# Kernel tuning notes

Hardware: AMD Instinct MI355X
Metric: run time of the kernel (lower is better)

The kernel has to match this reference:

```python
import jax, jax.numpy as jnp
import numpy as np

WS = 7   # w_size
K = 9    # k_neighbors


def setup_inputs() -> dict:
    key = jax.random.key(0)
    ks = jax.random.split(key, 6)
    B, C, H, W = 16, 64, 112, 112
    Cf = C // 4
    return {
        'x_in': jax.random.normal(ks[0], (B, C, H, W), jnp.float32),
        'Wf': jax.random.normal(ks[1], (Cf, C), jnp.float32) / np.sqrt(C).astype(np.float32),
        'bf': jnp.zeros((Cf,), jnp.float32),
        'Wp': jax.random.normal(ks[2], (C, Cf), jnp.float32) / np.sqrt(Cf).astype(np.float32),
        'bp': jnp.zeros((C,), jnp.float32),
        'W1': jax.random.normal(ks[3], (4, 2), jnp.float32) / np.sqrt(2.0).astype(np.float32),
        'b1': jnp.zeros((4,), jnp.float32),
        'W2': jax.random.normal(ks[4], (1, 4), jnp.float32) / 2.0,
        'b2': jnp.zeros((1,), jnp.float32),
        'sigma': jnp.asarray(4.0, jnp.float32),
        'alpha': jnp.asarray(0.5, jnp.float32),
    }


def reference(x_in, Wf, bf, Wp, bp, W1, b1, W2, b2, sigma, alpha):
    B, C, H, W = x_in.shape
    w, h = H // WS, W // WS                      # per-window spatial dims
    Bp, N = B * WS * WS, w * h                   # num windows, nodes per window
    # window partition: b c (Wg w) (Hg h) -> (b Wg Hg) c w h
    x = x_in.reshape(B, C, WS, w, WS, h).transpose(0, 2, 4, 1, 3, 5).reshape(Bp, C, w, h)
    # 1x1 conv f: dim -> dim//4
    f = jnp.einsum('bchw,oc->bohw', x, Wf) + bf[None, :, None, None]
    Cf = f.shape[1]
    xf = f.reshape(Bp, Cf, N).transpose(0, 2, 1)          # [Bp, N, Cf] node features
    # all-pairs cosine similarity (torch eps=1e-8)
    xn = xf / jnp.maximum(jnp.linalg.norm(xf, axis=-1, keepdims=True), 1e-8)
    sim_feat = jnp.einsum('bnc,bmc->bnm', xn, xn)         # [Bp, N, N]
    # spatial gaussian similarity
    ii, jj = jnp.meshgrid(jnp.arange(w), jnp.arange(h), indexing='ij')
    coords = jnp.stack([ii, jj], -1).reshape(N, 2).astype(jnp.float32)
    dist = jnp.sqrt(jnp.sum((coords[:, None] - coords[None]) ** 2, -1))
    sim_dist = jnp.exp(-dist ** 2 / (2.0 * sigma ** 2))   # [N, N]
    combined = alpha * sim_feat + (1.0 - alpha) * sim_dist[None]
    _, idx = jax.lax.top_k(combined, K)                   # [Bp, N, K] neighbor ids
    # gather neighbor messages; edges of node n are exactly its K top-k columns
    msg = xf[jnp.arange(Bp)[:, None, None], idx]          # [Bp, N, K, Cf]
    sf = jnp.take_along_axis(sim_feat, idx, axis=-1)      # edge cosine sim
    sd = sim_dist[jnp.arange(N)[:, None], idx]            # edge spatial sim
    pair = jnp.stack([sf, sd], -1)                        # [Bp, N, K, 2]
    hdn = jax.nn.silu(pair @ W1.T + b1)
    wgt = jax.nn.sigmoid(hdn @ W2.T + b2)[..., 0]         # [Bp, N, K]
    # scatter_add over edge_index[0] == per-source sum over its K edges
    wn = wgt / (jnp.sum(wgt, -1, keepdims=True) + 1e-12)
    out = jnp.einsum('bnk,bnkc->bnc', wn, msg)            # [Bp, N, Cf]
    out = out.reshape(Bp, w, h, Cf).transpose(0, 3, 1, 2)
    # window un-partition: (b Wg Hg) c w h -> b c (Wg w) (Hg h)
    out = out.reshape(B, WS, WS, Cf, w, h).transpose(0, 3, 1, 4, 2, 5).reshape(B, Cf, H, W)
    # 1x1 conv p: dim//4 -> dim, then flatten(2)
    y = jnp.einsum('bchw,oc->bohw', out, Wp) + bp[None, :, None, None]
    return y.reshape(B, C, H * W)
```

## Files before the change

kernel.cpp:

```cpp
#include <hip/hip_runtime.h>
#include <math.h>

#define CC    64
#define CF    16
#define NPIX  256
#define KK    9
#define HWQ   12544
#define WWQ   112
#define NTILE 784

__global__ __launch_bounds__(64, 4) void feat_k(
    const float* __restrict__ x_in, const float* __restrict__ Wf,
    const float* __restrict__ bf,
    float* __restrict__ xn_g, float* __restrict__ nrm_g)
{
    __shared__ float s_Wt[CC * CF];
    __shared__ float s_bf[CF];
    const int tid = threadIdx.x;
    for (int idx = tid; idx < CC * CF; idx += 64) {
        int c = idx >> 4, o = idx & 15;
        s_Wt[idx] = Wf[o * CC + c];
    }
    if (tid < CF) s_bf[tid] = bf[tid];
    __syncthreads();

    const int p    = blockIdx.x * 64 + tid;
    const int tile = p >> 8, pix = p & 255;
    const int bb = tile / 49, ssb = tile % 49;
    const int s1 = ssb / 7, s2 = ssb % 7;
    const int gy = s1 * 16 + (pix >> 4), gx = s2 * 16 + (pix & 15);
    const float* xb = x_in + (size_t)bb * CC * HWQ + (size_t)gy * WWQ + gx;

    float fv[CF];
    #pragma unroll
    for (int o = 0; o < CF; ++o) fv[o] = 0.0f;
    #pragma unroll 4
    for (int c = 0; c < CC; ++c) {
        float xv = xb[(size_t)c * HWQ];
        const float4* w4 = reinterpret_cast<const float4*>(&s_Wt[c << 4]);
        float4 w0 = w4[0], w1 = w4[1], w2 = w4[2], w3 = w4[3];
        fv[0]  = fmaf(xv, w0.x, fv[0]);  fv[1]  = fmaf(xv, w0.y, fv[1]);
        fv[2]  = fmaf(xv, w0.z, fv[2]);  fv[3]  = fmaf(xv, w0.w, fv[3]);
        fv[4]  = fmaf(xv, w1.x, fv[4]);  fv[5]  = fmaf(xv, w1.y, fv[5]);
        fv[6]  = fmaf(xv, w1.z, fv[6]);  fv[7]  = fmaf(xv, w1.w, fv[7]);
        fv[8]  = fmaf(xv, w2.x, fv[8]);  fv[9]  = fmaf(xv, w2.y, fv[9]);
        fv[10] = fmaf(xv, w2.z, fv[10]); fv[11] = fmaf(xv, w2.w, fv[11]);
        fv[12] = fmaf(xv, w3.x, fv[12]); fv[13] = fmaf(xv, w3.y, fv[13]);
        fv[14] = fmaf(xv, w3.z, fv[14]); fv[15] = fmaf(xv, w3.w, fv[15]);
    }
    #pragma unroll
    for (int o = 0; o < CF; ++o) fv[o] += s_bf[o];

    float ss2 = 0.0f;
    #pragma unroll
    for (int o = 0; o < CF; ++o) ss2 = fmaf(fv[o], fv[o], ss2);
    float nrm = fmaxf(sqrtf(ss2), 1e-8f);

    float xn[CF];
    #pragma unroll
    for (int o = 0; o < CF; ++o) xn[o] = fv[o] / nrm;

    float4* dst = reinterpret_cast<float4*>(xn_g + (size_t)p * CF);
    dst[0] = make_float4(xn[0],  xn[1],  xn[2],  xn[3]);
    dst[1] = make_float4(xn[4],  xn[5],  xn[6],  xn[7]);
    dst[2] = make_float4(xn[8],  xn[9],  xn[10], xn[11]);
    dst[3] = make_float4(xn[12], xn[13], xn[14], xn[15]);
    nrm_g[p] = nrm;
}

#define DOT16(dot, a0, a1, a2, a3)                                   \
    dot = fmaf(xnr[0],  (a0).x, dot); dot = fmaf(xnr[1],  (a0).y, dot); \
    dot = fmaf(xnr[2],  (a0).z, dot); dot = fmaf(xnr[3],  (a0).w, dot); \
    dot = fmaf(xnr[4],  (a1).x, dot); dot = fmaf(xnr[5],  (a1).y, dot); \
    dot = fmaf(xnr[6],  (a1).z, dot); dot = fmaf(xnr[7],  (a1).w, dot); \
    dot = fmaf(xnr[8],  (a2).x, dot); dot = fmaf(xnr[9],  (a2).y, dot); \
    dot = fmaf(xnr[10], (a2).z, dot); dot = fmaf(xnr[11], (a2).w, dot); \
    dot = fmaf(xnr[12], (a3).x, dot); dot = fmaf(xnr[13], (a3).y, dot); \
    dot = fmaf(xnr[14], (a3).z, dot); dot = fmaf(xnr[15], (a3).w, dot);

#define TOP9_INSERT(cv, ci) {                                        \
    const bool g0 = (cv) > tv0; const bool g1 = (cv) > tv1;          \
    const bool g2 = (cv) > tv2; const bool g3 = (cv) > tv3;          \
    const bool g4 = (cv) > tv4; const bool g5 = (cv) > tv5;          \
    const bool g6 = (cv) > tv6; const bool g7 = (cv) > tv7;          \
    const bool g8 = (cv) > tv8;                                      \
    const float nv0 = g0 ? (cv) : tv0;                               \
    const float nv1 = __builtin_amdgcn_fmed3f((cv), tv0, tv1);       \
    const float nv2 = __builtin_amdgcn_fmed3f((cv), tv1, tv2);       \
    const float nv3 = __builtin_amdgcn_fmed3f((cv), tv2, tv3);       \
    const float nv4 = __builtin_amdgcn_fmed3f((cv), tv3, tv4);       \
    const float nv5 = __builtin_amdgcn_fmed3f((cv), tv4, tv5);       \
    const float nv6 = __builtin_amdgcn_fmed3f((cv), tv5, tv6);       \
    const float nv7 = __builtin_amdgcn_fmed3f((cv), tv6, tv7);       \
    const float nv8 = __builtin_amdgcn_fmed3f((cv), tv7, tv8);       \
    const int nt0 = g0 ? (ci) : ti0;                                 \
    const int nt1 = g0 ? ti0 : (g1 ? (ci) : ti1);                    \
    const int nt2 = g1 ? ti1 : (g2 ? (ci) : ti2);                    \
    const int nt3 = g2 ? ti2 : (g3 ? (ci) : ti3);                    \
    const int nt4 = g3 ? ti3 : (g4 ? (ci) : ti4);                    \
    const int nt5 = g4 ? ti4 : (g5 ? (ci) : ti5);                    \
    const int nt6 = g5 ? ti5 : (g6 ? (ci) : ti6);                    \
    const int nt7 = g6 ? ti6 : (g7 ? (ci) : ti7);                    \
    const int nt8 = g7 ? ti7 : (g8 ? (ci) : ti8);                    \
    tv0 = nv0; tv1 = nv1; tv2 = nv2; tv3 = nv3; tv4 = nv4;           \
    tv5 = nv5; tv6 = nv6; tv7 = nv7; tv8 = nv8;                      \
    ti0 = nt0; ti1 = nt1; ti2 = nt2; ti3 = nt3; ti4 = nt4;           \
    ti5 = nt5; ti6 = nt6; ti7 = nt7; ti8 = nt8; }

#define SIM_ITER(MJ) {                                               \
    const int m = mbase + (MJ);                                      \
    const float4 a0 = c0, a1 = c1, a2 = c2, a3 = c3;                 \
    const float4* nx = reinterpret_cast<const float4*>(xt + (size_t)(m + 1) * CF); \
    c0 = nx[0]; c1 = nx[1]; c2 = nx[2]; c3 = nx[3];                  \
    float dot = 0.0f;                                                \
    DOT16(dot, a0, a1, a2, a3);                                      \
    const int dj = pj - (MJ);                                        \
    const float sdA = s_tabA[d2i + dj * dj];                         \
    const float comb = __fadd_rn(__fmul_rn(alpha, dot), sdA);        \
    TOP9_INSERT(comb, m); }

__global__ __launch_bounds__(64, 4) void gnn_main(
    const float* __restrict__ xn_g, const float* __restrict__ nrm_g,
    const float* __restrict__ Wp,   const float* __restrict__ bp,
    const float* __restrict__ W1,   const float* __restrict__ b1,
    const float* __restrict__ W2,   const float* __restrict__ b2,
    const float* __restrict__ sigma_p, const float* __restrict__ alpha_p,
    float* __restrict__ y)
{
    __shared__ float s_tab[451];
    __shared__ float s_tabA[451];
    __shared__ float s_Wp[CC * CF];
    __shared__ float s_bp[CC];

    const int bid  = blockIdx.x;
    const int tile = bid >> 2;
    const int rg   = bid & 3;
    const int bb = tile / 49, ssb = tile % 49;
    const int s1 = ssb / 7, s2 = ssb % 7;
    const int tid = threadIdx.x;

    const float alpha = alpha_p[0];
    const float oma   = 1.0f - alpha;
    const float sig   = sigma_p[0];
    const float denom = 2.0f * sig * sig;

    for (int t = tid; t < 451; t += 64) {
        float dd = sqrtf((float)t);
        float v  = expf((-(dd * dd)) / denom);
        s_tab[t]  = v;
        s_tabA[t] = __fmul_rn(oma, v);
    }
    for (int t = tid; t < CC * CF; t += 64) s_Wp[t] = Wp[t];
    s_bp[tid] = bp[tid];
    float W1r[8], b1r[4], W2r[4];
    #pragma unroll
    for (int h = 0; h < 8; ++h) W1r[h] = W1[h];
    #pragma unroll
    for (int h = 0; h < 4; ++h) { b1r[h] = b1[h]; W2r[h] = W2[h]; }
    const float b2r = b2[0];
    __syncthreads();

    const int r  = rg * 64 + tid;
    const int pi = r >> 4, pj = r & 15;
    const float* xt = xn_g + (size_t)tile * NPIX * CF;

    float xnr[CF];
    {
        const float4* xr4 = reinterpret_cast<const float4*>(xt + (size_t)r * CF);
        float4 r0 = xr4[0], r1 = xr4[1], r2 = xr4[2], r3 = xr4[3];
        xnr[0]=r0.x;  xnr[1]=r0.y;  xnr[2]=r0.z;  xnr[3]=r0.w;
        xnr[4]=r1.x;  xnr[5]=r1.y;  xnr[6]=r1.z;  xnr[7]=r1.w;
        xnr[8]=r2.x;  xnr[9]=r2.y;  xnr[10]=r2.z; xnr[11]=r2.w;
        xnr[12]=r3.x; xnr[13]=r3.y; xnr[14]=r3.z; xnr[15]=r3.w;
    }

    float tv0,tv1,tv2,tv3,tv4,tv5,tv6,tv7,tv8;
    int   ti0,ti1,ti2,ti3,ti4,ti5,ti6,ti7,ti8;
    tv0=tv1=tv2=tv3=tv4=tv5=tv6=tv7=tv8 = -INFINITY;
    ti0=ti1=ti2=ti3=ti4=ti5=ti6=ti7=ti8 = 0;

    float4 c0, c1, c2, c3;
    {
        const float4* p0 = reinterpret_cast<const float4*>(xt);
        c0 = p0[0]; c1 = p0[1]; c2 = p0[2]; c3 = p0[3];
    }

    #pragma unroll 1
    for (int mi = 0; mi < 16; ++mi) {
        const int di  = pi - mi;
        const int d2i = di * di;
        const int mbase = mi << 4;
        SIM_ITER(0)  SIM_ITER(1)  SIM_ITER(2)  SIM_ITER(3)
        SIM_ITER(4)  SIM_ITER(5)  SIM_ITER(6)  SIM_ITER(7)
        SIM_ITER(8)  SIM_ITER(9)  SIM_ITER(10) SIM_ITER(11)
        SIM_ITER(12) SIM_ITER(13) SIM_ITER(14) SIM_ITER(15)
    }

    const float tv[KK] = {tv0,tv1,tv2,tv3,tv4,tv5,tv6,tv7,tv8};
    const int   ti[KK] = {ti0,ti1,ti2,ti3,ti4,ti5,ti6,ti7,ti8};

    float wk[KK];
    float wsum = 0.0f;
    #pragma unroll
    for (int k = 0; k < KK; ++k) {
        int m = ti[k];
        int di = pi - (m >> 4);
        int dj = pj - (m & 15);
        float sd = s_tab[di * di + dj * dj];
        float sf = (tv[k] - __fmul_rn(oma, sd)) / alpha;
        float hsum = b2r;
        #pragma unroll
        for (int h = 0; h < 4; ++h) {
            float z  = fmaf(sf, W1r[2 * h], fmaf(sd, W1r[2 * h + 1], b1r[h]));
            float sg = 1.0f / (1.0f + expf(-z));
            hsum = fmaf(z * sg, W2r[h], hsum);
        }
        float wg = 1.0f / (1.0f + expf(-hsum));
        wk[k] = wg;
        wsum += wg;
    }
    wsum += 1e-12f;

    const float* nt = nrm_g + (size_t)tile * NPIX;
    float outv[CF];
    #pragma unroll
    for (int o = 0; o < CF; ++o) outv[o] = 0.0f;
    #pragma unroll
    for (int k = 0; k < KK; ++k) {
        const int m = ti[k];
        const float wnm = (wk[k] / wsum) * nt[m];
        const float4* xf4 = reinterpret_cast<const float4*>(xt + (size_t)m * CF);
        float4 m0 = xf4[0], m1 = xf4[1], m2 = xf4[2], m3 = xf4[3];
        outv[0]  = fmaf(wnm, m0.x, outv[0]);  outv[1]  = fmaf(wnm, m0.y, outv[1]);
        outv[2]  = fmaf(wnm, m0.z, outv[2]);  outv[3]  = fmaf(wnm, m0.w, outv[3]);
        outv[4]  = fmaf(wnm, m1.x, outv[4]);  outv[5]  = fmaf(wnm, m1.y, outv[5]);
        outv[6]  = fmaf(wnm, m1.z, outv[6]);  outv[7]  = fmaf(wnm, m1.w, outv[7]);
        outv[8]  = fmaf(wnm, m2.x, outv[8]);  outv[9]  = fmaf(wnm, m2.y, outv[9]);
        outv[10] = fmaf(wnm, m2.z, outv[10]); outv[11] = fmaf(wnm, m2.w, outv[11]);
        outv[12] = fmaf(wnm, m3.x, outv[12]); outv[13] = fmaf(wnm, m3.y, outv[13]);
        outv[14] = fmaf(wnm, m3.z, outv[14]); outv[15] = fmaf(wnm, m3.w, outv[15]);
    }

    const int gy = s1 * 16 + pi, gx = s2 * 16 + pj;
    float* yb = y + (size_t)bb * CC * HWQ + (size_t)gy * WWQ + gx;
    #pragma unroll 4
    for (int o = 0; o < CC; ++o) {
        const float4* w4 = reinterpret_cast<const float4*>(&s_Wp[o * CF]);
        float4 w0 = w4[0], w1 = w4[1], w2 = w4[2], w3 = w4[3];
        float acc = 0.0f;
        acc = fmaf(outv[0],  w0.x, acc); acc = fmaf(outv[1],  w0.y, acc);
        acc = fmaf(outv[2],  w0.z, acc); acc = fmaf(outv[3],  w0.w, acc);
        acc = fmaf(outv[4],  w1.x, acc); acc = fmaf(outv[5],  w1.y, acc);
        acc = fmaf(outv[6],  w1.z, acc); acc = fmaf(outv[7],  w1.w, acc);
        acc = fmaf(outv[8],  w2.x, acc); acc = fmaf(outv[9],  w2.y, acc);
        acc = fmaf(outv[10], w2.z, acc); acc = fmaf(outv[11], w2.w, acc);
        acc = fmaf(outv[12], w3.x, acc); acc = fmaf(outv[13], w3.y, acc);
        acc = fmaf(outv[14], w3.z, acc); acc = fmaf(outv[15], w3.w, acc);
        yb[(size_t)o * HWQ] = acc + s_bp[o];
    }
}

__global__ __launch_bounds__(256) void gnn_fused(
    const float* __restrict__ x_in, const float* __restrict__ Wf,
    const float* __restrict__ bf,   const float* __restrict__ Wp,
    const float* __restrict__ bp,   const float* __restrict__ W1,
    const float* __restrict__ b1,   const float* __restrict__ W2,
    const float* __restrict__ b2,   const float* __restrict__ sigma_p,
    const float* __restrict__ alpha_p, float* __restrict__ y)
{
    __shared__ float s_xf[NPIX][CF];
    __shared__ float s_xn[NPIX][CF];
    __shared__ float s_W[CC * CF];
    __shared__ float s_table[451];
    __shared__ float s_bias[CC];

    const int bpi = blockIdx.x;
    const int bb  = bpi / 49;
    const int ssb = bpi % 49;
    const int s1  = ssb / 7, s2 = ssb % 7;
    const int tid = threadIdx.x;
    const int pi  = tid >> 4, pj = tid & 15;
    const int gy  = s1 * 16 + pi, gx = s2 * 16 + pj;

    const float alpha = alpha_p[0];
    const float oma   = 1.0f - alpha;
    const float sig   = sigma_p[0];
    const float denom = 2.0f * sig * sig;

    for (int t = tid; t < CF * CC; t += NPIX) s_W[t] = Wf[t];
    if (tid < CF) s_bias[tid] = bf[tid];
    for (int t = tid; t < 451; t += NPIX) {
        float dd = sqrtf((float)t);
        s_table[t] = expf((-(dd * dd)) / denom);
    }
    float W1r[8], b1r[4], W2r[4];
    #pragma unroll
    for (int h = 0; h < 8; ++h) W1r[h] = W1[h];
    #pragma unroll
    for (int h = 0; h < 4; ++h) { b1r[h] = b1[h]; W2r[h] = W2[h]; }
    const float b2r = b2[0];
    __syncthreads();

    const float* xb = x_in + (size_t)bb * CC * HWQ + (size_t)gy * WWQ + gx;
    float fv[CF];
    #pragma unroll
    for (int o = 0; o < CF; ++o) fv[o] = 0.0f;
    for (int c = 0; c < CC; ++c) {
        float xv = xb[(size_t)c * HWQ];
        #pragma unroll
        for (int o = 0; o < CF; ++o)
            fv[o] = fmaf(xv, s_W[o * CC + c], fv[o]);
    }
    #pragma unroll
    for (int o = 0; o < CF; ++o) fv[o] += s_bias[o];

    float ss2 = 0.0f;
    #pragma unroll
    for (int o = 0; o < CF; ++o) ss2 = fmaf(fv[o], fv[o], ss2);
    float nrm = fmaxf(sqrtf(ss2), 1e-8f);

    float xnr[CF];
    #pragma unroll
    for (int o = 0; o < CF; ++o) {
        xnr[o] = fv[o] / nrm;
        s_xf[tid][o] = fv[o];
        s_xn[tid][o] = xnr[o];
    }
    __syncthreads();

    float tv[KK]; int ti[KK];
    #pragma unroll
    for (int k = 0; k < KK; ++k) { tv[k] = -INFINITY; ti[k] = 0; }

    for (int m = 0; m < NPIX; ++m) {
        const float4* xm4 = reinterpret_cast<const float4*>(&s_xn[m][0]);
        float4 a0 = xm4[0], a1 = xm4[1], a2 = xm4[2], a3 = xm4[3];
        float dot = 0.0f;
        dot = fmaf(xnr[0],  a0.x, dot); dot = fmaf(xnr[1],  a0.y, dot);
        dot = fmaf(xnr[2],  a0.z, dot); dot = fmaf(xnr[3],  a0.w, dot);
        dot = fmaf(xnr[4],  a1.x, dot); dot = fmaf(xnr[5],  a1.y, dot);
        dot = fmaf(xnr[6],  a1.z, dot); dot = fmaf(xnr[7],  a1.w, dot);
        dot = fmaf(xnr[8],  a2.x, dot); dot = fmaf(xnr[9],  a2.y, dot);
        dot = fmaf(xnr[10], a2.z, dot); dot = fmaf(xnr[11], a2.w, dot);
        dot = fmaf(xnr[12], a3.x, dot); dot = fmaf(xnr[13], a3.y, dot);
        dot = fmaf(xnr[14], a3.z, dot); dot = fmaf(xnr[15], a3.w, dot);

        int di = pi - (m >> 4);
        int dj = pj - (m & 15);
        float sd = s_table[di * di + dj * dj];
        float comb = __fadd_rn(__fmul_rn(alpha, dot), __fmul_rn(oma, sd));

        if (comb > tv[KK - 1]) {
            float cv = comb; int ci = m;
            #pragma unroll
            for (int t = KK - 1; t >= 0; --t) {
                bool g = (cv > tv[t]);
                float ov = tv[t]; int oi = ti[t];
                if (g) {
                    if (t + 1 < KK) { tv[t + 1] = ov; ti[t + 1] = oi; }
                    tv[t] = cv; ti[t] = ci;
                }
            }
        }
    }

    float wk[KK];
    float wsum = 0.0f;
    #pragma unroll
    for (int k = 0; k < KK; ++k) {
        int m = ti[k];
        int di = pi - (m >> 4);
        int dj = pj - (m & 15);
        float sd = s_table[di * di + dj * dj];
        float sf = (tv[k] - __fmul_rn(oma, sd)) / alpha;
        float hsum = b2r;
        #pragma unroll
        for (int h = 0; h < 4; ++h) {
            float z  = fmaf(sf, W1r[2 * h], fmaf(sd, W1r[2 * h + 1], b1r[h]));
            float sg = 1.0f / (1.0f + expf(-z));
            hsum = fmaf(z * sg, W2r[h], hsum);
        }
        float wg = 1.0f / (1.0f + expf(-hsum));
        wk[k] = wg;
        wsum += wg;
    }
    wsum += 1e-12f;

    float outv[CF];
    #pragma unroll
    for (int o = 0; o < CF; ++o) outv[o] = 0.0f;
    #pragma unroll
    for (int k = 0; k < KK; ++k) {
        float wn = wk[k] / wsum;
        int m = ti[k];
        const float4* xf4 = reinterpret_cast<const float4*>(&s_xf[m][0]);
        float4 m0 = xf4[0], m1 = xf4[1], m2 = xf4[2], m3 = xf4[3];
        outv[0]  = fmaf(wn, m0.x, outv[0]);  outv[1]  = fmaf(wn, m0.y, outv[1]);
        outv[2]  = fmaf(wn, m0.z, outv[2]);  outv[3]  = fmaf(wn, m0.w, outv[3]);
        outv[4]  = fmaf(wn, m1.x, outv[4]);  outv[5]  = fmaf(wn, m1.y, outv[5]);
        outv[6]  = fmaf(wn, m1.z, outv[6]);  outv[7]  = fmaf(wn, m1.w, outv[7]);
        outv[8]  = fmaf(wn, m2.x, outv[8]);  outv[9]  = fmaf(wn, m2.y, outv[9]);
        outv[10] = fmaf(wn, m2.z, outv[10]); outv[11] = fmaf(wn, m2.w, outv[11]);
        outv[12] = fmaf(wn, m3.x, outv[12]); outv[13] = fmaf(wn, m3.y, outv[13]);
        outv[14] = fmaf(wn, m3.z, outv[14]); outv[15] = fmaf(wn, m3.w, outv[15]);
    }

    __syncthreads();
    for (int t = tid; t < CC * CF; t += NPIX) s_W[t] = Wp[t];
    if (tid < CC) s_bias[tid] = bp[tid];
    __syncthreads();

    float* yb = y + (size_t)bb * CC * HWQ + (size_t)gy * WWQ + gx;
    for (int o = 0; o < CC; ++o) {
        float acc = 0.0f;
        #pragma unroll
        for (int c = 0; c < CF; ++c)
            acc = fmaf(outv[c], s_W[o * CF + c], acc);
        yb[(size_t)o * HWQ] = acc + s_bias[o];
    }
}

extern "C" void kernel_launch(void* const* d_in, const int* in_sizes, int n_in,
                              void* d_out, int out_size, void* d_ws, size_t ws_size,
                              hipStream_t stream) {
    const float* x_in  = (const float*)d_in[0];
    const float* Wf    = (const float*)d_in[1];
    const float* bf    = (const float*)d_in[2];
    const float* Wp    = (const float*)d_in[3];
    const float* bp    = (const float*)d_in[4];
    const float* W1    = (const float*)d_in[5];
    const float* b1    = (const float*)d_in[6];
    const float* W2    = (const float*)d_in[7];
    const float* b2    = (const float*)d_in[8];
    const float* sigma = (const float*)d_in[9];
    const float* alpha = (const float*)d_in[10];
    float* y = (float*)d_out;

    const size_t need = (size_t)(NTILE * NPIX * CF + NTILE * NPIX) * sizeof(float);
    if (ws_size >= need) {
        float* xn_g  = (float*)d_ws;
        float* nrm_g = xn_g + (size_t)NTILE * NPIX * CF;
        feat_k<<<3136, 64, 0, stream>>>(x_in, Wf, bf, xn_g, nrm_g);
        gnn_main<<<3136, 64, 0, stream>>>(xn_g, nrm_g, Wp, bp, W1, b1, W2, b2,
                                          sigma, alpha, y);
    } else {
        gnn_fused<<<NTILE, NPIX, 0, stream>>>(x_in, Wf, bf, Wp, bp, W1, b1, W2,
                                              b2, sigma, alpha, y);
    }
}
```

Baseline: 160.8 us.

## Stage window node features in LDS and use 128-thread blocks for gnn_main

gnn_main now copies each window's 256x16 normalized features and norms into shared memory once per block. The all-pairs similarity loop, the neighbour gather and the norm lookups then read from LDS instead of global/L2. Blocks grow from 64 to 128 threads, with two blocks per tile instead of four. The Wp and bp projection weights move out of LDS and are read directly from global memory, and feat_k's channel loop unroll goes from 4 to 8. The change trades roughly 17KB of LDS per block, which may limit occupancy, for fewer global loads in the hot O(N^2) loop.

```diff
diff --git a/kernel.cpp b/kernel.cpp
--- a/kernel.cpp
+++ b/kernel.cpp
@@ -8,6 +8,7 @@
 #define HWQ   12544
 #define WWQ   112
 #define NTILE 784
+#define MBLK  128
 
 __global__ __launch_bounds__(64, 4) void feat_k(
     const float* __restrict__ x_in, const float* __restrict__ Wf,
@@ -34,7 +35,7 @@
     float fv[CF];
     #pragma unroll
     for (int o = 0; o < CF; ++o) fv[o] = 0.0f;
-    #pragma unroll 4
+    #pragma unroll 8
     for (int c = 0; c < CC; ++c) {
         float xv = xb[(size_t)c * HWQ];
         const float4* w4 = reinterpret_cast<const float4*>(&s_Wt[c << 4]);
@@ -109,9 +110,8 @@
 
 #define SIM_ITER(MJ) {                                               \
     const int m = mbase + (MJ);                                      \
-    const float4 a0 = c0, a1 = c1, a2 = c2, a3 = c3;                 \
-    const float4* nx = reinterpret_cast<const float4*>(xt + (size_t)(m + 1) * CF); \
-    c0 = nx[0]; c1 = nx[1]; c2 = nx[2]; c3 = nx[3];                  \
+    const float4* xm4 = reinterpret_cast<const float4*>(&s_xn[m][0]);\
+    const float4 a0 = xm4[0], a1 = xm4[1], a2 = xm4[2], a3 = xm4[3]; \
     float dot = 0.0f;                                                \
     DOT16(dot, a0, a1, a2, a3);                                      \
     const int dj = pj - (MJ);                                        \
@@ -119,7 +119,7 @@
     const float comb = __fadd_rn(__fmul_rn(alpha, dot), sdA);        \
     TOP9_INSERT(comb, m); }
 
-__global__ __launch_bounds__(64, 4) void gnn_main(
+__global__ __launch_bounds__(MBLK, 4) void gnn_main(
     const float* __restrict__ xn_g, const float* __restrict__ nrm_g,
     const float* __restrict__ Wp,   const float* __restrict__ bp,
     const float* __restrict__ W1,   const float* __restrict__ b1,
@@ -127,14 +127,14 @@
     const float* __restrict__ sigma_p, const float* __restrict__ alpha_p,
     float* __restrict__ y)
 {
+    __shared__ float s_xn[NPIX][CF];
+    __shared__ float s_nrm[NPIX];
     __shared__ float s_tab[451];
     __shared__ float s_tabA[451];
-    __shared__ float s_Wp[CC * CF];
-    __shared__ float s_bp[CC];
 
     const int bid  = blockIdx.x;
-    const int tile = bid >> 2;
-    const int rg   = bid & 3;
+    const int tile = bid >> 1;
+    const int hlf  = bid & 1;
     const int bb = tile / 49, ssb = tile % 49;
     const int s1 = ssb / 7, s2 = ssb % 7;
     const int tid = threadIdx.x;
@@ -144,14 +144,22 @@
     const float sig   = sigma_p[0];
     const float denom = 2.0f * sig * sig;
 
-    for (int t = tid; t < 451; t += 64) {
+    for (int t = tid; t < 451; t += MBLK) {
         float dd = sqrtf((float)t);
         float v  = expf((-(dd * dd)) / denom);
         s_tab[t]  = v;
         s_tabA[t] = __fmul_rn(oma, v);
     }
-    for (int t = tid; t < CC * CF; t += 64) s_Wp[t] = Wp[t];
-    s_bp[tid] = bp[tid];
+    const float* xt = xn_g + (size_t)tile * NPIX * CF;
+    {
+        const float4* src = reinterpret_cast<const float4*>(xt);
+        float4*       dst = reinterpret_cast<float4*>(&s_xn[0][0]);
+        #pragma unroll
+        for (int i = 0; i < 8; ++i) dst[tid + i * MBLK] = src[tid + i * MBLK];
+        const float* nsrc = nrm_g + (size_t)tile * NPIX;
+        s_nrm[tid]        = nsrc[tid];
+        s_nrm[tid + MBLK] = nsrc[tid + MBLK];
+    }
     float W1r[8], b1r[4], W2r[4];
     #pragma unroll
     for (int h = 0; h < 8; ++h) W1r[h] = W1[h];
@@ -160,13 +168,12 @@
     const float b2r = b2[0];
     __syncthreads();
 
-    const int r  = rg * 64 + tid;
+    const int r  = hlf * MBLK + tid;
     const int pi = r >> 4, pj = r & 15;
-    const float* xt = xn_g + (size_t)tile * NPIX * CF;
 
     float xnr[CF];
     {
-        const float4* xr4 = reinterpret_cast<const float4*>(xt + (size_t)r * CF);
+        const float4* xr4 = reinterpret_cast<const float4*>(&s_xn[r][0]);
         float4 r0 = xr4[0], r1 = xr4[1], r2 = xr4[2], r3 = xr4[3];
         xnr[0]=r0.x;  xnr[1]=r0.y;  xnr[2]=r0.z;  xnr[3]=r0.w;
         xnr[4]=r1.x;  xnr[5]=r1.y;  xnr[6]=r1.z;  xnr[7]=r1.w;
@@ -178,12 +185,6 @@
     int   ti0,ti1,ti2,ti3,ti4,ti5,ti6,ti7,ti8;
     tv0=tv1=tv2=tv3=tv4=tv5=tv6=tv7=tv8 = -INFINITY;
     ti0=ti1=ti2=ti3=ti4=ti5=ti6=ti7=ti8 = 0;
-
-    float4 c0, c1, c2, c3;
-    {
-        const float4* p0 = reinterpret_cast<const float4*>(xt);
-        c0 = p0[0]; c1 = p0[1]; c2 = p0[2]; c3 = p0[3];
-    }
 
     #pragma unroll 1
     for (int mi = 0; mi < 16; ++mi) {
@@ -221,15 +222,14 @@
     }
     wsum += 1e-12f;
 
-    const float* nt = nrm_g + (size_t)tile * NPIX;
     float outv[CF];
     #pragma unroll
     for (int o = 0; o < CF; ++o) outv[o] = 0.0f;
     #pragma unroll
     for (int k = 0; k < KK; ++k) {
         const int m = ti[k];
-        const float wnm = (wk[k] / wsum) * nt[m];
-        const float4* xf4 = reinterpret_cast<const float4*>(xt + (size_t)m * CF);
+        const float wnm = (wk[k] / wsum) * s_nrm[m];
+        const float4* xf4 = reinterpret_cast<const float4*>(&s_xn[m][0]);
         float4 m0 = xf4[0], m1 = xf4[1], m2 = xf4[2], m3 = xf4[3];
         outv[0]  = fmaf(wnm, m0.x, outv[0]);  outv[1]  = fmaf(wnm, m0.y, outv[1]);
         outv[2]  = fmaf(wnm, m0.z, outv[2]);  outv[3]  = fmaf(wnm, m0.w, outv[3]);
@@ -245,7 +245,7 @@
     float* yb = y + (size_t)bb * CC * HWQ + (size_t)gy * WWQ + gx;
     #pragma unroll 4
     for (int o = 0; o < CC; ++o) {
-        const float4* w4 = reinterpret_cast<const float4*>(&s_Wp[o * CF]);
+        const float4* w4 = reinterpret_cast<const float4*>(&Wp[o * CF]);
         float4 w0 = w4[0], w1 = w4[1], w2 = w4[2], w3 = w4[3];
         float acc = 0.0f;
         acc = fmaf(outv[0],  w0.x, acc); acc = fmaf(outv[1],  w0.y, acc);
@@ -256,7 +256,7 @@
         acc = fmaf(outv[10], w2.z, acc); acc = fmaf(outv[11], w2.w, acc);
         acc = fmaf(outv[12], w3.x, acc); acc = fmaf(outv[13], w3.y, acc);
         acc = fmaf(outv[14], w3.z, acc); acc = fmaf(outv[15], w3.w, acc);
-        yb[(size_t)o * HWQ] = acc + s_bp[o];
+        yb[(size_t)o * HWQ] = acc + bp[o];
     }
 }
 
@@ -441,8 +441,8 @@
         float* xn_g  = (float*)d_ws;
         float* nrm_g = xn_g + (size_t)NTILE * NPIX * CF;
         feat_k<<<3136, 64, 0, stream>>>(x_in, Wf, bf, xn_g, nrm_g);
-        gnn_main<<<3136, 64, 0, stream>>>(xn_g, nrm_g, Wp, bp, W1, b1, W2, b2,
-                                          sigma, alpha, y);
+        gnn_main<<<NTILE * 2, MBLK, 0, stream>>>(xn_g, nrm_g, Wp, bp, W1, b1,
+                                                 W2, b2, sigma, alpha, y);
     } else {
         gnn_fused<<<NTILE, NPIX, 0, stream>>>(x_in, Wf, bf, Wp, bp, W1, b1, W2,
                                               b2, sigma, alpha, y);
```

After: 131.1 us. -18.4%, faster.
